# Kernel tuning notes

Measured on AMD Instinct MI355X. Metric: run time of the kernel, lower is better.

Reference implementation:

```python
import jax, jax.numpy as jnp
import numpy as np

T, D, S, Q, K = 768, 24, 576, 32, 128   # tokens, dense atoms/token, subsets, queries/subset, keys/subset
CA, CP, CT, H, DH = 128, 16, 384, 4, 32  # per-atom ch, pair ch, per-token ch, heads, head dim


def _conv_feat(idx, arr):
    # atom_layout.convert with layout_axes=(-3,-2): flatten first two axes, gather, keep channels
    return arr.reshape(-1, arr.shape[-1])[idx]


def _conv_flat(idx, arr):
    # atom_layout.convert with layout_axes=(-2,-1): flatten all layout axes, gather
    return arr.reshape(-1)[idx]


def setup_inputs() -> dict:
    key = jax.random.key(0)
    ks = iter(jax.random.split(key, 64))

    def nrm(shape, scale=0.05):
        return jax.random.normal(next(ks), shape, dtype=jnp.float32) * scale

    inp = {}
    inp["ref_positions"] = nrm((T, D, 3), 1.0)
    inp["ref_mask"] = jnp.ones((T, D), jnp.float32)
    inp["ref_charge"] = nrm((T, D), 1.0)
    inp["atom_mask"] = jnp.ones((T, D), jnp.float32)
    inp["ref_element"] = jax.random.randint(next(ks), (T, D), 0, 128)
    inp["ref_atom_name_chars"] = jax.random.randint(next(ks), (T, D, 4), 0, 64)
    inp["ref_space_uid"] = jax.random.randint(next(ks), (T, D), 0, T)
    inp["t2q_idx"] = jax.random.randint(next(ks), (S, Q), 0, T * D)
    inp["q2k_idx"] = jax.random.randint(next(ks), (S, K), 0, S * Q)
    inp["q2t_idx"] = jax.random.randint(next(ks), (T, D), 0, S * Q)
    # learned weights (stored (in, out); y = x @ W, equivalent to torch Linear with W.T)
    inp["w_ref_pos"] = nrm((3, CA))
    inp["w_ref_mask"] = nrm((1, CA))
    inp["w_ref_element"] = nrm((128, CA))
    inp["w_ref_charge"] = nrm((1, CA))
    inp["w_ref_atom_name"] = nrm((256, CA))
    inp["w_s2p_row1"] = nrm((CA, CP))
    inp["w_s2p_col1"] = nrm((CA, CP))
    inp["w_pair_off1"] = nrm((3, CP))
    inp["w_pair_dist1"] = nrm((1, CP))
    inp["w_pair_valid"] = nrm((1, CP))
    inp["w_mlp1"] = nrm((CP, CP))
    inp["w_mlp2"] = nrm((CP, CP))
    inp["w_mlp3"] = nrm((CP, CP))
    inp["wq"] = nrm((CA, H * DH))
    inp["wk"] = nrm((CA, H * DH))
    inp["wv"] = nrm((CA, H * DH))
    inp["wb"] = nrm((CP, H))
    inp["wo"] = nrm((H * DH, CA))
    inp["w_proj"] = nrm((CA, CT))
    return inp


def reference(ref_positions, ref_mask, ref_charge, atom_mask,
              ref_element, ref_atom_name_chars, ref_space_uid,
              t2q_idx, q2k_idx, q2t_idx,
              w_ref_pos, w_ref_mask, w_ref_element, w_ref_charge, w_ref_atom_name,
              w_s2p_row1, w_s2p_col1, w_pair_off1, w_pair_dist1, w_pair_valid,
              w_mlp1, w_mlp2, w_mlp3, wq, wk, wv, wb, wo, w_proj):
    # ---- per-atom conditioning ----
    act = ref_positions @ w_ref_pos                                   # (T,D,CA)
    act += ref_mask[..., None] @ w_ref_mask
    act += jax.nn.one_hot(ref_element, 128, dtype=jnp.float32) @ w_ref_element
    act += jnp.arcsinh(ref_charge)[..., None] @ w_ref_charge
    name_1hot = jax.nn.one_hot(ref_atom_name_chars, 64, dtype=jnp.float32).reshape(T, D, 256)
    act += name_1hot @ w_ref_atom_name
    act *= ref_mask[..., None]

    # ---- layout conversions (gathers) ----
    queries_single_cond = _conv_feat(t2q_idx, act)                    # (S,Q,CA)
    queries_mask = _conv_flat(t2q_idx, atom_mask)                     # (S,Q)
    queries_act = queries_single_cond
    keys_single_cond = _conv_feat(q2k_idx, queries_single_cond)       # (S,K,CA)
    keys_mask = _conv_flat(q2k_idx, queries_mask)                     # (S,K)

    # ---- pair conditioning: broadcast row+col, offsets, inv-sq-dist, validity ----
    row1 = jax.nn.relu(queries_single_cond) @ w_s2p_row1              # (S,Q,CP)
    col1 = jax.nn.relu(keys_single_cond) @ w_s2p_col1                 # (S,K,CP)
    pair = row1[:, :, None, :] + col1[:, None, :, :]                  # (S,Q,K,CP)

    queries_ref_pos = _conv_feat(t2q_idx, ref_positions)              # (S,Q,3)
    queries_uid = _conv_flat(t2q_idx, ref_space_uid)                  # (S,Q)
    keys_ref_pos = _conv_feat(q2k_idx, queries_ref_pos)               # (S,K,3)
    keys_uid = _conv_flat(q2k_idx, ref_space_uid)                     # (S,K)

    valid = (queries_uid[:, :, None] == keys_uid[:, None, :])         # (S,Q,K)
    validf = valid[..., None].astype(jnp.float32)
    offsets = queries_ref_pos[:, :, None, :] - keys_ref_pos[:, None, :, :]  # (S,Q,K,3)
    pair += (offsets @ w_pair_off1) * validf
    sq_dists = jnp.sum(jnp.square(offsets), axis=-1)
    pair += ((1.0 / (1.0 + sq_dists))[..., None] @ w_pair_dist1) * validf
    pair += validf @ w_pair_valid

    p2 = jax.nn.relu(pair) @ w_mlp1
    p2 = jax.nn.relu(p2) @ w_mlp2
    pair += jax.nn.relu(p2) @ w_mlp3

    # ---- cross-attention (queries attend to keys, pair_cond as bias) ----
    keys_act = _conv_feat(q2k_idx, queries_act)                       # (S,K,CA)
    q = (queries_act @ wq).reshape(S, Q, H, DH)
    k = (keys_act @ wk).reshape(S, K, H, DH)
    v = (keys_act @ wv).reshape(S, K, H, DH)
    bias = pair @ wb                                                  # (S,Q,K,H)
    logits = jnp.einsum('sqhd,skhd->sqkh', q, k) / jnp.sqrt(jnp.float32(DH)) + bias
    logits = jnp.where(keys_mask[:, None, :, None] > 0, logits, jnp.float32(-1e9))
    attn = jax.nn.softmax(logits, axis=2)
    o = jnp.einsum('sqkh,skhd->sqhd', attn, v).reshape(S, Q, H * DH)
    queries_act = queries_act + o @ wo

    queries_act = queries_act * queries_mask[..., None]
    skip_connection = queries_act
    proj = queries_act @ w_proj                                       # (S,Q,CT)
    token_atoms_act = _conv_feat(q2t_idx, proj)                       # (T,D,CT)

    # mask_mean over dense atom axis
    num = jnp.sum(atom_mask[..., None] * jax.nn.relu(token_atoms_act), axis=-2)
    den = jnp.sum(atom_mask, axis=-1, keepdims=True) + 1e-10
    token_act = num / den                                             # (T,CT)

    return (token_act, skip_connection, queries_mask, queries_single_cond,
            keys_mask, keys_single_cond, pair)
```

## Files before the change

### kernel.cpp

```cpp
#include <hip/hip_runtime.h>

typedef unsigned short u16;
typedef unsigned int u32;

#define T_ 768
#define D_ 24
#define S_ 576
#define Q_ 32
#define K_ 128
#define CA_ 128
#define CP_ 16
#define CT_ 384
#define H_ 4
#define DH_ 32
#define SQ_ (S_*Q_)
#define SK_ (S_*K_)

__device__ __forceinline__ float b2f(u16 u){ return __uint_as_float(((u32)u)<<16); }
__device__ __forceinline__ u16 f2b(float f){ u32 x=__float_as_uint(f); return (u16)((x + 0x7fffu + ((x>>16)&1u))>>16); }

__global__ __launch_bounds__(128) void n_qsc(
    const float* __restrict__ pos, const float* __restrict__ rmask, const float* __restrict__ charge,
    const float* __restrict__ amask, const int* __restrict__ elem, const int* __restrict__ chars,
    const int* __restrict__ uid, const int* __restrict__ t2q,
    const float* __restrict__ w_pos, const float* __restrict__ w_mask, const float* __restrict__ w_elem,
    const float* __restrict__ w_chg, const float* __restrict__ w_name,
    float* __restrict__ qsc, float* __restrict__ qmask, float* __restrict__ qrp, int* __restrict__ quid,
    float* __restrict__ out_qsc, float* __restrict__ out_qmask)
{
  int slot = blockIdx.x, ch = threadIdx.x;
  int a = t2q[slot];
  float p0 = pos[a*3+0], p1 = pos[a*3+1], p2 = pos[a*3+2];
  float m  = rmask[a];
  float cg = asinhf(charge[a]);
  int e  = elem[a];
  int c0 = chars[a*4+0], c1 = chars[a*4+1], c2 = chars[a*4+2], c3 = chars[a*4+3];
  float v = p0*w_pos[0*CA_+ch] + p1*w_pos[1*CA_+ch] + p2*w_pos[2*CA_+ch];
  v += m * w_mask[ch];
  v += w_elem[e*CA_+ch];
  v += cg * w_chg[ch];
  v += w_name[(0*64+c0)*CA_+ch] + w_name[(1*64+c1)*CA_+ch]
     + w_name[(2*64+c2)*CA_+ch] + w_name[(3*64+c3)*CA_+ch];
  v *= m;
  qsc[(size_t)slot*CA_+ch] = v;
  out_qsc[(size_t)slot*CA_+ch] = v;
  if (ch < 3) qrp[slot*3+ch] = pos[a*3+ch];
  if (ch == 0){
    float am = amask[a];
    qmask[slot] = am;
    out_qmask[slot] = am;
    quid[slot] = uid[a];
  }
}

__global__ __launch_bounds__(128) void n_keys(
    const float* __restrict__ qsc, const float* __restrict__ qmask, const float* __restrict__ qrp,
    const int* __restrict__ uid, const int* __restrict__ q2k,
    float* __restrict__ krp, int* __restrict__ kuid,
    float* __restrict__ out_ksc, float* __restrict__ out_kmask)
{
  int sk = blockIdx.x, ch = threadIdx.x;
  int j = q2k[sk];
  out_ksc[(size_t)sk*CA_+ch] = qsc[(size_t)j*CA_+ch];
  if (ch < 3) krp[sk*3+ch] = qrp[j*3+ch];
  if (ch == 0){
    out_kmask[sk] = qmask[j];
    kuid[sk] = uid[j];
  }
}

__global__ __launch_bounds__(128) void n_qkv(
    const float* __restrict__ X, const float* __restrict__ wq, const float* __restrict__ wk,
    const float* __restrict__ wv, float* __restrict__ Qp, float* __restrict__ Kp, float* __restrict__ Vp)
{
  __shared__ float Xs[16*CA_];
  int tid = threadIdx.x;
  size_t r0 = (size_t)blockIdx.x * 16;
  for (int e = tid; e < 16*CA_; e += 128) Xs[e] = X[r0*CA_ + e];
  __syncthreads();
  int c = tid;
  float acc[16];

  #pragma unroll
  for (int r = 0; r < 16; ++r) acc[r] = 0.f;
  for (int i = 0; i < CA_; ++i){
    float w = wq[i*CA_+c];
    #pragma unroll
    for (int r = 0; r < 16; ++r) acc[r] += Xs[r*CA_+i] * w;
  }
  #pragma unroll
  for (int r = 0; r < 16; ++r) Qp[(r0+r)*CA_+c] = acc[r] * 0.17677669529663687f;

  #pragma unroll
  for (int r = 0; r < 16; ++r) acc[r] = 0.f;
  for (int i = 0; i < CA_; ++i){
    float w = wk[i*CA_+c];
    #pragma unroll
    for (int r = 0; r < 16; ++r) acc[r] += Xs[r*CA_+i] * w;
  }
  #pragma unroll
  for (int r = 0; r < 16; ++r) Kp[(r0+r)*CA_+c] = acc[r];

  #pragma unroll
  for (int r = 0; r < 16; ++r) acc[r] = 0.f;
  for (int i = 0; i < CA_; ++i){
    float w = wv[i*CA_+c];
    #pragma unroll
    for (int r = 0; r < 16; ++r) acc[r] += Xs[r*CA_+i] * w;
  }
  #pragma unroll
  for (int r = 0; r < 16; ++r) Vp[(r0+r)*CA_+c] = acc[r];
}

__global__ __launch_bounds__(128) void n_proj16(
    const float* __restrict__ X, const float* __restrict__ W, float* __restrict__ Y)
{
  int row = blockIdx.x*8 + (threadIdx.x >> 4);
  int c = threadIdx.x & 15;
  float acc = 0.f;
  for (int i = 0; i < CA_; ++i)
    acc += fmaxf(X[(size_t)row*CA_+i], 0.f) * W[i*CP_+c];
  Y[(size_t)row*CP_+c] = acc;
}

__global__ __launch_bounds__(128) void n_pair(
    const int* __restrict__ q2k, const float* __restrict__ rowproj, const float* __restrict__ colproj,
    const float* __restrict__ qrp, const int* __restrict__ quid,
    const float* __restrict__ krp, const int* __restrict__ kuid,
    const float* __restrict__ w1, const float* __restrict__ w2, const float* __restrict__ w3,
    const float* __restrict__ wpo, const float* __restrict__ wpd, const float* __restrict__ wpv,
    const float* __restrict__ wb,
    float* __restrict__ out_pair, u16* __restrict__ bias_ws)
{
  __shared__ float w1s[256], w2s[256], w3s[256], wbs[64], wpos[48], wpds[16], wpvs[16];
  int tid = threadIdx.x;
  for (int e = tid; e < 256; e += 128){ w1s[e] = w1[e]; w2s[e] = w2[e]; w3s[e] = w3[e]; }
  if (tid < 64) wbs[tid] = wb[tid];
  if (tid < 48) wpos[tid] = wpo[tid];
  if (tid < 16){ wpds[tid] = wpd[tid]; wpvs[tid] = wpv[tid]; }
  __syncthreads();

  int sq = blockIdx.x;
  int s  = sq >> 5;
  int k  = tid;
  int sk = s*K_ + k;
  int j  = q2k[sk];

  float p[16];
  {
    float ox = qrp[sq*3+0] - krp[sk*3+0];
    float oy = qrp[sq*3+1] - krp[sk*3+1];
    float oz = qrp[sq*3+2] - krp[sk*3+2];
    float vf = (quid[sq] == kuid[sk]) ? 1.f : 0.f;
    float invd = vf / (1.f + ox*ox + oy*oy + oz*oz);
    #pragma unroll
    for (int c = 0; c < 16; ++c)
      p[c] = rowproj[(size_t)sq*CP_+c] + colproj[(size_t)j*CP_+c]
           + vf*(ox*wpos[c] + oy*wpos[16+c] + oz*wpos[32+c])
           + invd*wpds[c] + vf*wpvs[c];
  }
  float y[16];
  #pragma unroll
  for (int c = 0; c < 16; ++c) y[c] = 0.f;
  for (int i = 0; i < 16; ++i){
    float u = fmaxf(p[i], 0.f);
    #pragma unroll
    for (int c = 0; c < 16; ++c) y[c] += u * w1s[i*16+c];
  }
  float z[16];
  #pragma unroll
  for (int c = 0; c < 16; ++c) z[c] = 0.f;
  for (int i = 0; i < 16; ++i){
    float u = fmaxf(y[i], 0.f);
    #pragma unroll
    for (int c = 0; c < 16; ++c) z[c] += u * w2s[i*16+c];
  }
  for (int i = 0; i < 16; ++i){
    float u = fmaxf(z[i], 0.f);
    #pragma unroll
    for (int c = 0; c < 16; ++c) p[c] += u * w3s[i*16+c];
  }
  float b[4] = {0.f, 0.f, 0.f, 0.f};
  for (int c = 0; c < 16; ++c){
    #pragma unroll
    for (int h = 0; h < 4; ++h) b[h] += p[c] * wbs[c*4+h];
  }
  size_t rg = (size_t)sq*K_ + k;
  for (int c = 0; c < 16; ++c) out_pair[rg*16+c] = p[c];
  for (int h = 0; h < 4; ++h)  bias_ws[rg*4+h] = f2b(b[h]);
}

__global__ __launch_bounds__(128) void n_attn(
    const float* __restrict__ Qp, const float* __restrict__ Kp, const float* __restrict__ Vp,
    const float* __restrict__ qmask, const u16* __restrict__ bias_ws, const int* __restrict__ q2k,
    float* __restrict__ O)
{
  __shared__ float Ks[128*36];
  __shared__ float Vs[128*36];
  __shared__ float msk[128];
  __shared__ float redm[64];
  __shared__ float reds[64];
  __shared__ float Osm[32*33];

  int b = blockIdx.x;
  int s = b >> 2, h = b & 3;
  int sq0 = s * Q_;
  int base = s * K_;
  int t = threadIdx.x;

  {
    int e = t & 7, rr = t >> 3;
    #pragma unroll
    for (int it = 0; it < 8; ++it){
      int row = it*16 + rr;
      int j = q2k[base + row];
      const float4* ksrc = (const float4*)&Kp[(size_t)j*CA_ + h*DH_];
      const float4* vsrc = (const float4*)&Vp[(size_t)j*CA_ + h*DH_];
      *(float4*)&Ks[row*36 + e*4] = ksrc[e];
      *(float4*)&Vs[row*36 + e*4] = vsrc[e];
    }
    int j0 = q2k[base + t];
    msk[t] = qmask[j0];
  }

  int q  = t & 31;
  int kr = t >> 5;
  float qreg[32];
  {
    const float4* qsrc = (const float4*)&Qp[(size_t)(sq0+q)*CA_ + h*DH_];
    #pragma unroll
    for (int d4 = 0; d4 < 8; ++d4){
      float4 v = qsrc[d4];
      qreg[d4*4+0] = v.x; qreg[d4*4+1] = v.y; qreg[d4*4+2] = v.z; qreg[d4*4+3] = v.w;
    }
  }
  __syncthreads();

  float p[32];
  #pragma unroll
  for (int kk = 0; kk < 32; ++kk){
    int k = kr*32 + kk;
    const float* kbase = &Ks[k*36];
    float acc = 0.f;
    #pragma unroll
    for (int d4 = 0; d4 < 8; ++d4){
      float4 kv = *(const float4*)(kbase + d4*4);
      acc += qreg[d4*4+0]*kv.x + qreg[d4*4+1]*kv.y + qreg[d4*4+2]*kv.z + qreg[d4*4+3]*kv.w;
    }
    float bz = b2f(bias_ws[((size_t)(sq0+q)*K_ + k)*4 + h]);
    p[kk] = (msk[k] > 0.f) ? (acc + bz) : -1e9f;
  }

  float m = p[0];
  #pragma unroll
  for (int kk = 1; kk < 32; ++kk) m = fmaxf(m, p[kk]);
  m = fmaxf(m, __shfl_xor(m, 32, 64));
  int wv = t >> 6;
  if ((t & 63) < 32) redm[wv*32 + q] = m;
  __syncthreads();
  float M = fmaxf(redm[q], redm[32 + q]);

  float sm = 0.f;
  #pragma unroll
  for (int kk = 0; kk < 32; ++kk){ p[kk] = __expf(p[kk] - M); sm += p[kk]; }
  sm += __shfl_xor(sm, 32, 64);
  if ((t & 63) < 32) reds[wv*32 + q] = sm;
  __syncthreads();
  float inv = 1.f / (reds[q] + reds[32 + q]);

  float acc[32];
  #pragma unroll
  for (int d = 0; d < 32; ++d) acc[d] = 0.f;
  #pragma unroll
  for (int kk = 0; kk < 32; ++kk){
    float w = p[kk];
    const float* vbase = &Vs[(kr*32 + kk)*36];
    #pragma unroll
    for (int d4 = 0; d4 < 8; ++d4){
      float4 vv = *(const float4*)(vbase + d4*4);
      acc[d4*4+0] += w*vv.x; acc[d4*4+1] += w*vv.y; acc[d4*4+2] += w*vv.z; acc[d4*4+3] += w*vv.w;
    }
  }
  #pragma unroll
  for (int d = 0; d < 32; ++d) acc[d] += __shfl_xor(acc[d], 32, 64);
  if (t < 32){
    #pragma unroll
    for (int d = 0; d < 32; ++d) Osm[q*33 + d] = acc[d];
  }
  __syncthreads();
  if (t >= 64 && t < 96){
    #pragma unroll
    for (int d = 0; d < 32; ++d) Osm[q*33 + d] = (Osm[q*33 + d] + acc[d]) * inv;
  }
  __syncthreads();

  #pragma unroll
  for (int it = 0; it < 2; ++it){
    int idx = it*128 + t;
    int qq = idx >> 3, e = idx & 7;
    float4 v = make_float4(Osm[qq*33 + e*4 + 0], Osm[qq*33 + e*4 + 1],
                           Osm[qq*33 + e*4 + 2], Osm[qq*33 + e*4 + 3]);
    *(float4*)&O[(size_t)(sq0+qq)*CA_ + h*DH_ + e*4] = v;
  }
}

__global__ __launch_bounds__(128) void n_qact(
    const float* __restrict__ qsc, const float* __restrict__ O, const float* __restrict__ qmask,
    const float* __restrict__ wo, float* __restrict__ qact, float* __restrict__ out_skip)
{
  __shared__ float Os[16*CA_];
  int tid = threadIdx.x;
  size_t r0 = (size_t)blockIdx.x * 16;
  for (int e = tid; e < 16*CA_; e += 128) Os[e] = O[r0*CA_ + e];
  __syncthreads();
  int c = tid;
  float acc[16];
  #pragma unroll
  for (int r = 0; r < 16; ++r) acc[r] = 0.f;
  for (int i = 0; i < CA_; ++i){
    float w = wo[i*CA_+c];
    #pragma unroll
    for (int r = 0; r < 16; ++r) acc[r] += Os[r*CA_+i] * w;
  }
  #pragma unroll
  for (int r = 0; r < 16; ++r){
    float v = (qsc[(r0+r)*CA_+c] + acc[r]) * qmask[r0+r];
    qact[(r0+r)*CA_+c] = v;
    out_skip[(r0+r)*CA_+c] = v;
  }
}

__global__ __launch_bounds__(384) void n_tok(
    const float* __restrict__ qact, const int* __restrict__ q2t, const float* __restrict__ amask,
    const float* __restrict__ wp, float* __restrict__ out_tok)
{
  __shared__ float Xs[D_*CA_];
  __shared__ int   jr[D_];
  __shared__ float mk[D_];
  int t = blockIdx.x, tid = threadIdx.x;
  if (tid < D_){
    jr[tid] = q2t[t*D_ + tid];
    mk[tid] = amask[t*D_ + tid];
  }
  __syncthreads();
  for (int e = tid; e < D_*CA_; e += 384){
    int d = e >> 7, i = e & 127;
    Xs[e] = qact[(size_t)jr[d]*CA_ + i];
  }
  __syncthreads();
  int ct = tid;
  float acc[D_];
  #pragma unroll
  for (int d = 0; d < D_; ++d) acc[d] = 0.f;
  for (int i = 0; i < CA_; ++i){
    float w = wp[i*CT_ + ct];
    #pragma unroll
    for (int d = 0; d < D_; ++d) acc[d] += Xs[d*CA_ + i] * w;
  }
  float num = 0.f, den = 1e-10f;
  #pragma unroll
  for (int d = 0; d < D_; ++d){
    num += mk[d] * fmaxf(acc[d], 0.f);
    den += mk[d];
  }
  out_tok[(size_t)t*CT_ + ct] = num/den;
}

extern "C" void kernel_launch(void* const* d_in, const int* in_sizes, int n_in,
                              void* d_out, int out_size, void* d_ws, size_t ws_size,
                              hipStream_t stream) {
  (void)in_sizes; (void)n_in; (void)out_size; (void)ws_size;
  const float* ref_positions = (const float*)d_in[0];
  const float* ref_mask      = (const float*)d_in[1];
  const float* ref_charge    = (const float*)d_in[2];
  const float* atom_mask     = (const float*)d_in[3];
  const int*   ref_element   = (const int*)d_in[4];
  const int*   ref_chars     = (const int*)d_in[5];
  const int*   ref_uid       = (const int*)d_in[6];
  const int*   t2q           = (const int*)d_in[7];
  const int*   q2k           = (const int*)d_in[8];
  const int*   q2t           = (const int*)d_in[9];
  const float* w_ref_pos     = (const float*)d_in[10];
  const float* w_ref_mask    = (const float*)d_in[11];
  const float* w_ref_element = (const float*)d_in[12];
  const float* w_ref_charge  = (const float*)d_in[13];
  const float* w_ref_name    = (const float*)d_in[14];
  const float* w_s2p_row1    = (const float*)d_in[15];
  const float* w_s2p_col1    = (const float*)d_in[16];
  const float* w_pair_off1   = (const float*)d_in[17];
  const float* w_pair_dist1  = (const float*)d_in[18];
  const float* w_pair_valid  = (const float*)d_in[19];
  const float* w_mlp1        = (const float*)d_in[20];
  const float* w_mlp2        = (const float*)d_in[21];
  const float* w_mlp3        = (const float*)d_in[22];
  const float* wq            = (const float*)d_in[23];
  const float* wk            = (const float*)d_in[24];
  const float* wv            = (const float*)d_in[25];
  const float* wb            = (const float*)d_in[26];
  const float* wo            = (const float*)d_in[27];
  const float* w_proj        = (const float*)d_in[28];

  char* ws = (char*)d_ws;
  float* qsc     = (float*)(ws + 0);
  float* qmask   = (float*)(ws + 9437184);
  float* qrp     = (float*)(ws + 9732096);
  int*   quid    = (int*)  (ws + 9953280);
  float* krp     = (float*)(ws + 10027008);
  int*   kuid    = (int*)  (ws + 10911744);
  float* rowproj = (float*)(ws + 11206656);
  float* colproj = (float*)(ws + 12386304);
  float* Qp      = (float*)(ws + 13565952);
  float* Kp      = (float*)(ws + 23003136);
  float* Vp      = (float*)(ws + 32440320);
  float* O       = (float*)(ws + 41877504);
  float* qact    = (float*)(ws + 51314688);
  u16*   biasws  = (u16*)  (ws + 60751872);

  float* out = (float*)d_out;
  float* out_tok   = out + 0;
  float* out_skip  = out + 294912;
  float* out_qmask = out + 2654208;
  float* out_qsc   = out + 2672640;
  float* out_kmask = out + 5031936;
  float* out_ksc   = out + 5105664;
  float* out_pair  = out + 14542848;

  hipLaunchKernelGGL(n_qsc, dim3(SQ_), dim3(128), 0, stream,
      ref_positions, ref_mask, ref_charge, atom_mask, ref_element, ref_chars, ref_uid, t2q,
      w_ref_pos, w_ref_mask, w_ref_element, w_ref_charge, w_ref_name,
      qsc, qmask, qrp, quid, out_qsc, out_qmask);
  hipLaunchKernelGGL(n_keys, dim3(SK_), dim3(128), 0, stream,
      qsc, qmask, qrp, ref_uid, q2k, krp, kuid, out_ksc, out_kmask);
  hipLaunchKernelGGL(n_qkv, dim3(SQ_/16), dim3(128), 0, stream,
      qsc, wq, wk, wv, Qp, Kp, Vp);
  hipLaunchKernelGGL(n_proj16, dim3(SQ_/8), dim3(128), 0, stream,
      qsc, w_s2p_row1, rowproj);
  hipLaunchKernelGGL(n_proj16, dim3(SQ_/8), dim3(128), 0, stream,
      qsc, w_s2p_col1, colproj);
  hipLaunchKernelGGL(n_pair, dim3(SQ_), dim3(128), 0, stream,
      q2k, rowproj, colproj, qrp, quid, krp, kuid,
      w_mlp1, w_mlp2, w_mlp3, w_pair_off1, w_pair_dist1, w_pair_valid, wb,
      out_pair, biasws);
  hipLaunchKernelGGL(n_attn, dim3(S_*H_), dim3(128), 0, stream,
      Qp, Kp, Vp, qmask, biasws, q2k, O);
  hipLaunchKernelGGL(n_qact, dim3(SQ_/16), dim3(128), 0, stream,
      qsc, O, qmask, wo, qact, out_skip);
  hipLaunchKernelGGL(n_tok, dim3(T_), dim3(384), 0, stream,
      qact, q2t, atom_mask, w_proj, out_tok);
}
```

Measured before the change: 614.6 us.

## Coalesce pair output stores, transpose bias layout, vectorize key gather, fuse projections

New measurement: 596.5 us. -2.9%, faster.

```diff
diff --git a/kernel.cpp b/kernel.cpp
--- a/kernel.cpp
+++ b/kernel.cpp
@@ -59,11 +59,13 @@
     float* __restrict__ krp, int* __restrict__ kuid,
     float* __restrict__ out_ksc, float* __restrict__ out_kmask)
 {
-  int sk = blockIdx.x, ch = threadIdx.x;
+  int r = threadIdx.x >> 5;
+  int e = threadIdx.x & 31;
+  int sk = blockIdx.x*4 + r;
   int j = q2k[sk];
-  out_ksc[(size_t)sk*CA_+ch] = qsc[(size_t)j*CA_+ch];
-  if (ch < 3) krp[sk*3+ch] = qrp[j*3+ch];
-  if (ch == 0){
+  *(float4*)&out_ksc[(size_t)sk*CA_ + e*4] = *(const float4*)&qsc[(size_t)j*CA_ + e*4];
+  if (e < 3) krp[sk*3+e] = qrp[j*3+e];
+  if (e == 0){
     out_kmask[sk] = qmask[j];
     kuid[sk] = uid[j];
   }
@@ -112,15 +114,19 @@
   for (int r = 0; r < 16; ++r) Vp[(r0+r)*CA_+c] = acc[r];
 }
 
-__global__ __launch_bounds__(128) void n_proj16(
-    const float* __restrict__ X, const float* __restrict__ W, float* __restrict__ Y)
-{
-  int row = blockIdx.x*8 + (threadIdx.x >> 4);
-  int c = threadIdx.x & 15;
+__global__ __launch_bounds__(128) void n_proj16b(
+    const float* __restrict__ X, const float* __restrict__ Wr, const float* __restrict__ Wc,
+    float* __restrict__ Yr, float* __restrict__ Yc)
+{
+  int row = blockIdx.x*4 + (threadIdx.x >> 5);
+  int c = threadIdx.x & 31;
+  const float* W = (c < 16) ? Wr : Wc;
+  float* Y = (c < 16) ? Yr : Yc;
+  int cc = c & 15;
   float acc = 0.f;
   for (int i = 0; i < CA_; ++i)
-    acc += fmaxf(X[(size_t)row*CA_+i], 0.f) * W[i*CP_+c];
-  Y[(size_t)row*CP_+c] = acc;
+    acc += fmaxf(X[(size_t)row*CA_+i], 0.f) * W[i*CP_+cc];
+  Y[(size_t)row*CP_+cc] = acc;
 }
 
 __global__ __launch_bounds__(128) void n_pair(
@@ -133,6 +139,7 @@
     float* __restrict__ out_pair, u16* __restrict__ bias_ws)
 {
   __shared__ float w1s[256], w2s[256], w3s[256], wbs[64], wpos[48], wpds[16], wpvs[16];
+  __shared__ __align__(16) float Ls[128*20];
   int tid = threadIdx.x;
   for (int e = tid; e < 256; e += 128){ w1s[e] = w1[e]; w2s[e] = w2[e]; w3s[e] = w3[e]; }
   if (tid < 64) wbs[tid] = wb[tid];
@@ -142,9 +149,20 @@
 
   int sq = blockIdx.x;
   int s  = sq >> 5;
+  int q  = sq & 31;
   int k  = tid;
   int sk = s*K_ + k;
   int j  = q2k[sk];
+
+  float rp[16], cp[16];
+  *(float4*)&rp[0]  = *(const float4*)&rowproj[(size_t)sq*CP_ + 0];
+  *(float4*)&rp[4]  = *(const float4*)&rowproj[(size_t)sq*CP_ + 4];
+  *(float4*)&rp[8]  = *(const float4*)&rowproj[(size_t)sq*CP_ + 8];
+  *(float4*)&rp[12] = *(const float4*)&rowproj[(size_t)sq*CP_ + 12];
+  *(float4*)&cp[0]  = *(const float4*)&colproj[(size_t)j*CP_ + 0];
+  *(float4*)&cp[4]  = *(const float4*)&colproj[(size_t)j*CP_ + 4];
+  *(float4*)&cp[8]  = *(const float4*)&colproj[(size_t)j*CP_ + 8];
+  *(float4*)&cp[12] = *(const float4*)&colproj[(size_t)j*CP_ + 12];
 
   float p[16];
   {
@@ -155,7 +173,7 @@
     float invd = vf / (1.f + ox*ox + oy*oy + oz*oz);
     #pragma unroll
     for (int c = 0; c < 16; ++c)
-      p[c] = rowproj[(size_t)sq*CP_+c] + colproj[(size_t)j*CP_+c]
+      p[c] = rp[c] + cp[c]
            + vf*(ox*wpos[c] + oy*wpos[16+c] + oz*wpos[32+c])
            + invd*wpds[c] + vf*wpvs[c];
   }
@@ -185,9 +203,22 @@
     #pragma unroll
     for (int h = 0; h < 4; ++h) b[h] += p[c] * wbs[c*4+h];
   }
-  size_t rg = (size_t)sq*K_ + k;
-  for (int c = 0; c < 16; ++c) out_pair[rg*16+c] = p[c];
-  for (int h = 0; h < 4; ++h)  bias_ws[rg*4+h] = f2b(b[h]);
+
+  #pragma unroll
+  for (int h = 0; h < 4; ++h)
+    bias_ws[(((size_t)s*H_ + h)*Q_ + q)*K_ + k] = f2b(b[h]);
+
+  #pragma unroll
+  for (int c4 = 0; c4 < 4; ++c4)
+    *(float4*)&Ls[k*20 + c4*4] = make_float4(p[c4*4+0], p[c4*4+1], p[c4*4+2], p[c4*4+3]);
+  __syncthreads();
+  size_t obase = (size_t)sq * (K_*CP_);
+  #pragma unroll
+  for (int i = 0; i < 4; ++i){
+    int g4 = i*128 + tid;
+    int kk = g4 >> 2, c = (g4 & 3)*4;
+    *(float4*)&out_pair[obase + (size_t)g4*4] = *(const float4*)&Ls[kk*20 + c];
+  }
 }
 
 __global__ __launch_bounds__(128) void n_attn(
@@ -234,6 +265,16 @@
       qreg[d4*4+0] = v.x; qreg[d4*4+1] = v.y; qreg[d4*4+2] = v.z; qreg[d4*4+3] = v.w;
     }
   }
+
+  u32 bw[16];
+  {
+    const uint4* bsrc = (const uint4*)&bias_ws[(((size_t)s*H_ + h)*Q_ + q)*K_ + kr*32];
+    uint4 B;
+    B = bsrc[0]; bw[0]=B.x;  bw[1]=B.y;  bw[2]=B.z;  bw[3]=B.w;
+    B = bsrc[1]; bw[4]=B.x;  bw[5]=B.y;  bw[6]=B.z;  bw[7]=B.w;
+    B = bsrc[2]; bw[8]=B.x;  bw[9]=B.y;  bw[10]=B.z; bw[11]=B.w;
+    B = bsrc[3]; bw[12]=B.x; bw[13]=B.y; bw[14]=B.z; bw[15]=B.w;
+  }
   __syncthreads();
 
   float p[32];
@@ -247,7 +288,7 @@
       float4 kv = *(const float4*)(kbase + d4*4);
       acc += qreg[d4*4+0]*kv.x + qreg[d4*4+1]*kv.y + qreg[d4*4+2]*kv.z + qreg[d4*4+3]*kv.w;
     }
-    float bz = b2f(bias_ws[((size_t)(sq0+q)*K_ + k)*4 + h]);
+    float bz = b2f((u16)((bw[kk>>1] >> ((kk&1)*16)) & 0xffffu));
     p[kk] = (msk[k] > 0.f) ? (acc + bz) : -1e9f;
   }
 
@@ -429,14 +470,12 @@
       ref_positions, ref_mask, ref_charge, atom_mask, ref_element, ref_chars, ref_uid, t2q,
       w_ref_pos, w_ref_mask, w_ref_element, w_ref_charge, w_ref_name,
       qsc, qmask, qrp, quid, out_qsc, out_qmask);
-  hipLaunchKernelGGL(n_keys, dim3(SK_), dim3(128), 0, stream,
+  hipLaunchKernelGGL(n_keys, dim3(SK_/4), dim3(128), 0, stream,
       qsc, qmask, qrp, ref_uid, q2k, krp, kuid, out_ksc, out_kmask);
   hipLaunchKernelGGL(n_qkv, dim3(SQ_/16), dim3(128), 0, stream,
       qsc, wq, wk, wv, Qp, Kp, Vp);
-  hipLaunchKernelGGL(n_proj16, dim3(SQ_/8), dim3(128), 0, stream,
-      qsc, w_s2p_row1, rowproj);
-  hipLaunchKernelGGL(n_proj16, dim3(SQ_/8), dim3(128), 0, stream,
-      qsc, w_s2p_col1, colproj);
+  hipLaunchKernelGGL(n_proj16b, dim3(SQ_/4), dim3(128), 0, stream,
+      qsc, w_s2p_row1, w_s2p_col1, rowproj, colproj);
   hipLaunchKernelGGL(n_pair, dim3(SQ_), dim3(128), 0, stream,
       q2k, rowproj, colproj, qrp, quid, krp, kuid,
       w_mlp1, w_mlp2, w_mlp3, w_pair_off1, w_pair_dist1, w_pair_valid, wb,
```
